# Kernel optimization log

Hardware: AMD Instinct MI355X
Metric: run time of the kernel (lower is better)

The kernel has to match this reference:

```python
import jax, jax.numpy as jnp
import numpy as np

D_TOK = 1222
N_BOU = 80

def _pe(n, d):
    pos = np.arange(n, dtype=np.float32)[:, None]
    div = np.exp(np.arange(0, d, 2, dtype=np.float32) * (-np.log(10000.0) / d))
    pe = np.zeros((n, d), np.float32)
    pe[:, 0::2] = np.sin(pos * div)
    pe[:, 1::2] = np.cos(pos * div)
    return jnp.asarray(pe)

def _ln(x, g, b, eps=1e-5):
    m = jnp.mean(x, -1, keepdims=True)
    v = jnp.mean((x - m) ** 2, -1, keepdims=True)
    return (x - m) / jnp.sqrt(v + eps) * g + b

_gather = jax.vmap(lambda f, i: f[:, i[..., 0], i[..., 1]])  # f [C,H,W], i [...,2] -> [C,...]


def setup_inputs() -> dict:
    key = jax.random.key(0)
    ks = jax.random.split(key, 8)
    D, FF, N = D_TOK, 2048, N_BOU
    s = 0.02
    return {
        "curr_img_features": jax.random.normal(ks[0], (2, 1024, 224, 224), jnp.float32),
        "previous_boundary": jax.random.randint(ks[1], (2, N, 2), 0, 224, dtype=jnp.int32),
        "ln_g": jnp.ones((D,), jnp.float32), "ln_b": jnp.zeros((D,), jnp.float32),
        "in_proj_w": s * jax.random.normal(ks[2], (3 * D, D), jnp.float32),
        "in_proj_b": jnp.zeros((3 * D,), jnp.float32),
        "out_proj_w": s * jax.random.normal(ks[3], (D, D), jnp.float32),
        "out_proj_b": jnp.zeros((D,), jnp.float32),
        "lin1_w": s * jax.random.normal(ks[4], (FF, D), jnp.float32),
        "lin1_b": jnp.zeros((FF,), jnp.float32),
        "lin2_w": s * jax.random.normal(ks[5], (D, FF), jnp.float32),
        "lin2_b": jnp.zeros((D,), jnp.float32),
        "norm1_g": jnp.ones((D,), jnp.float32), "norm1_b": jnp.zeros((D,), jnp.float32),
        "norm2_g": jnp.ones((D,), jnp.float32), "norm2_b": jnp.zeros((D,), jnp.float32),
        "fc_w": s * jax.random.normal(ks[6], (N, 1026, D), jnp.float32),
        "fc_b": jnp.zeros((N, 1026), jnp.float32),
    }


def reference(curr_img_features, previous_boundary, ln_g, ln_b, in_proj_w, in_proj_b,
              out_proj_w, out_proj_b, lin1_w, lin1_b, lin2_w, lin2_b,
              norm1_g, norm1_b, norm2_g, norm2_b, fc_w, fc_b):
    D = D_TOK
    offs = jnp.array([[dx, dy] for dx in range(-3, 4) for dy in range(-3, 4)], jnp.int32)  # [49,2]
    # multi-scale avg-pooled + zero-padded maps (hoisted out of the refine loop; identical math)
    padded = []
    for s in range(4):
        k = 2 ** s
        f = curr_img_features
        if k > 1:
            B, C, H, W = f.shape
            f = f.reshape(B, C, H // k, k, W // k, k).mean((3, 5))
        padded.append(jnp.pad(f, ((0, 0), (0, 0), (3, 3), (3, 3))))
    pe = _pe(N_BOU, D)
    boundary = previous_boundary.astype(jnp.int32)
    results = []
    for _ in range(6):
        qf = _gather(curr_img_features, boundary)  # [B,C,N]
        dots = []
        for s in range(4):
            bs = boundary // (2 ** s)
            idx = bs[:, :, None, :] + offs[None, None] + 3  # [B,N,49,2] into padded map
            keyf = _gather(padded[s], idx)  # [B,C,N,49]
            dots.append(jnp.einsum('bcn,bcno->bno', qf, keyf))
        dots = jnp.concatenate(dots, axis=2)  # [B,N,196]
        tokens = jnp.concatenate([qf.transpose(0, 2, 1), dots,
                                  boundary.astype(jnp.float32)], axis=2)  # [B,N,1222]
        tokens = _ln(tokens, ln_g, ln_b)
        tokens = tokens + pe[None]  # positional encoding (dropout = eval/identity)
        # TransformerEncoderLayer, nhead=1, post-norm, relu, no dropout (eval)
        qkv = tokens @ in_proj_w.T + in_proj_b
        q, k_, v = jnp.split(qkv, 3, axis=-1)
        sc = jnp.einsum('bnd,bmd->bnm', q, k_) / jnp.sqrt(jnp.float32(D))
        attn = jax.nn.softmax(sc, axis=-1) @ v
        attn = attn @ out_proj_w.T + out_proj_b
        x = _ln(tokens + attn, norm1_g, norm1_b)
        ff = jax.nn.relu(x @ lin1_w.T + lin1_b) @ lin2_w.T + lin2_b
        x = _ln(x + ff, norm2_g, norm2_b)
        # 80 independent per-token heads, batched
        out = jnp.einsum('bnd,nod->bno', x, fc_w) + fc_b[None]  # [B,80,1026]
        off_f = out[..., :2]
        # torch .long() truncates toward zero; clip keeps gathers in-range (original clamp was a no-op bug)
        boundary = jnp.clip(boundary + jnp.trunc(off_f).astype(jnp.int32), 0, 223)
        results.append(boundary)
    return jnp.stack(results)  # [6,B,80,2] int32
```

## Files before the change

kernel.cpp:

```cpp
#include <hip/hip_runtime.h>
#include <math.h>

#define DTOK 1222
#define NBOU 80
#define MM   160
#define FFD  2048
#define OQKV 3666

typedef __attribute__((ext_vector_type(8))) short short8;
typedef __attribute__((ext_vector_type(4))) float f32x4;

__device__ __forceinline__ unsigned short f2bf(float x) {
  unsigned int u = __float_as_uint(x);
  unsigned int r = (u + 0x7FFFu + ((u >> 16) & 1u)) >> 16;
  return (unsigned short)r;
}
__device__ __forceinline__ float bf2f(unsigned short h) {
  return __uint_as_float((unsigned int)h << 16);
}

__device__ __forceinline__ float wave_red_sum(float v) {
#pragma unroll
  for (int off = 32; off; off >>= 1) v += __shfl_xor(v, off, 64);
  return v;
}
__device__ __forceinline__ float block_red_sum(float v, float* rb, int tid) {
  v = wave_red_sum(v);
  __syncthreads();
  if ((tid & 63) == 0) rb[tid >> 6] = v;
  __syncthreads();
  return rb[0] + rb[1] + rb[2] + rb[3];
}

__device__ __forceinline__ void frag_write_row(const float* __restrict__ row,
                                               short* __restrict__ Af,
                                               int r, int T, int tid) {
  int mt = r >> 6, mf = (r >> 4) & 3, rl = r & 15;
  for (int task = tid; task < T * 4; task += 256) {
    int t = task >> 2, kq = task & 3;
    const float* src = row + t * 32 + kq * 8;
    short8 h, l, q;
#pragma unroll
    for (int j = 0; j < 8; ++j) {
      float x = src[j];
      unsigned short hb = f2bf(x);
      float r1 = x - bf2f(hb);
      unsigned short lb = f2bf(r1);
      float r2 = r1 - bf2f(lb);
      h[j] = (short)hb; l[j] = (short)lb; q[j] = (short)f2bf(r2);
    }
    size_t base = (size_t)(mt * T + t) * 6144 + mf * 512 + (size_t)(rl + kq * 16) * 8;
    *(short8*)(Af + base) = h;
    *(short8*)(Af + base + 2048) = l;
    *(short8*)(Af + base + 4096) = q;
  }
}

__global__ __launch_bounds__(256) void k_nhwc0p(const float* __restrict__ f,
                                                float* __restrict__ L0n,
                                                float* __restrict__ L1) {
  int xt = blockIdx.x;
  int y1 = blockIdx.y;
  int zc = blockIdx.z;
  int b = zc >> 5, ct = zc & 31;
  __shared__ float tile[32][65];
  int tid = threadIdx.x;
  const float* fb = f + (size_t)b * 1024 * 50176;
#pragma unroll
  for (int i = 0; i < 8; ++i) {
    int u = tid + 256 * i;
    int xl = u & 31, r = (u >> 5) & 1, c = u >> 6;
    tile[c][xl + 32 * r] = fb[(size_t)(ct * 32 + c) * 50176 +
                              (size_t)(2 * y1 + r) * 224 + xt * 32 + xl];
  }
  __syncthreads();
#pragma unroll
  for (int i = 0; i < 8; ++i) {
    int u = tid + 256 * i;
    int c2 = u & 31, x2 = (u >> 5) & 31, r2 = u >> 10;
    L0n[(((size_t)b * 224 + 2 * y1 + r2) * 224 + xt * 32 + x2) * 1024 + ct * 32 + c2] =
        tile[c2][x2 + 32 * r2];
  }
#pragma unroll
  for (int i = 0; i < 2; ++i) {
    int u = tid + 256 * i;
    int c3 = u & 31, xp = u >> 5;
    float v = 0.25f * (tile[c3][2 * xp] + tile[c3][2 * xp + 1] +
                       tile[c3][32 + 2 * xp] + tile[c3][32 + 2 * xp + 1]);
    L1[(((size_t)b * 112 + y1) * 112 + xt * 16 + xp) * 1024 + ct * 32 + c3] = v;
  }
}

__global__ __launch_bounds__(256) void k_pool_nhwc(const float* __restrict__ in,
                                                   float* __restrict__ out, int Ho) {
  int x = blockIdx.x, y = blockIdx.y, b = blockIdx.z;
  int c = threadIdx.x * 4;
  int Hi = Ho * 2;
  const float* p00 = in + (((size_t)(b * Hi + 2 * y) * Hi) + 2 * x) * 1024 + c;
  const float* p01 = p00 + 1024;
  const float* p10 = p00 + (size_t)Hi * 1024;
  const float* p11 = p10 + 1024;
  float4 a = *(const float4*)p00, bv = *(const float4*)p01;
  float4 cv = *(const float4*)p10, dv = *(const float4*)p11;
  float4 r;
  r.x = 0.25f * (a.x + bv.x + cv.x + dv.x);
  r.y = 0.25f * (a.y + bv.y + cv.y + dv.y);
  r.z = 0.25f * (a.z + bv.z + cv.z + dv.z);
  r.w = 0.25f * (a.w + bv.w + cv.w + dv.w);
  *(float4*)(out + (((size_t)(b * Ho + y) * Ho) + x) * 1024 + c) = r;
}

__global__ __launch_bounds__(256) void k_pe(float* __restrict__ pe, int* __restrict__ bnd,
                                            const int* __restrict__ pb) {
  int n = blockIdx.x, tid = threadIdx.x;
  for (int d = tid; d < DTOK; d += 256) {
    int i = d >> 1;
    double e = exp((double)(2 * i) * (-log(10000.0) / (double)DTOK));
    double ang = (double)n * e;
    pe[n * DTOK + d] = (float)((d & 1) ? cos(ang) : sin(ang));
  }
  if (n == 0) {
    for (int t = tid; t < 2 * NBOU * 2; t += 256) bnd[t] = pb[t];
  }
}

__global__ __launch_bounds__(256) void k_conv(const float* __restrict__ X,
                                              short* __restrict__ F,
                                              int R, int K, int T) {
  int b = blockIdx.x;
  int rt = b / T, t = b % T;
  int tid = threadIdx.x, mf = tid >> 6, lane = tid & 63;
  int row = rt * 64 + mf * 16 + (lane & 15);
  int k0 = t * 32 + (lane >> 4) * 8;
  float a[8];
#pragma unroll
  for (int j = 0; j < 8; ++j) {
    int k = k0 + j;
    a[j] = (row < R && k < K) ? X[(size_t)row * K + k] : 0.f;
  }
  short8 h, l, q;
#pragma unroll
  for (int j = 0; j < 8; ++j) {
    float x = a[j];
    unsigned short hb = f2bf(x);
    float r1 = x - bf2f(hb);
    unsigned short lb = f2bf(r1);
    float r2 = r1 - bf2f(lb);
    h[j] = (short)hb; l[j] = (short)lb; q[j] = (short)f2bf(r2);
  }
  size_t base = (size_t)b * 6144 + mf * 512 + (size_t)lane * 8;
  *(short8*)(F + base) = h;
  *(short8*)(F + base + 2048) = l;
  *(short8*)(F + base + 4096) = q;
}

__global__ __launch_bounds__(256) void k_dots(const float* __restrict__ L0n,
                                              const float* __restrict__ L1,
                                              const float* __restrict__ L2,
                                              const float* __restrict__ L3,
                                              const int* __restrict__ bnd,
                                              float* __restrict__ dots) {
  int o = blockIdx.x;
  int blk = blockIdx.y;
  int b = blk / NBOU;
  int tid = threadIdx.x, s = tid >> 6, lane = tid & 63;
  int bd0 = bnd[blk * 2 + 0], bd1 = bnd[blk * 2 + 1];
  const float* cp = L0n + (((size_t)b * 224 + bd0) * 224 + bd1) * 1024;
  int Hs = 224 >> s;
  const float* base = (s == 0) ? L0n : (s == 1) ? L1 : (s == 2) ? L2 : L3;
  int yy = (bd0 >> s) + o / 7 - 3;
  int xx = (bd1 >> s) + o % 7 - 3;
  float a = 0.f;
  if (yy >= 0 && yy < Hs && xx >= 0 && xx < Hs) {
    const float* kp = base + (((size_t)b * Hs + yy) * Hs + xx) * 1024;
#pragma unroll
    for (int j = 0; j < 4; ++j) {
      int c = (lane + 64 * j) * 4;
      float4 kv = *(const float4*)(kp + c);
      float4 qv = *(const float4*)(cp + c);
      a += kv.x * qv.x + kv.y * qv.y + kv.z * qv.z + kv.w * qv.w;
    }
  }
  a = wave_red_sum(a);
  if (lane == 0) dots[blk * 196 + s * 49 + o] = a;
}

__global__ __launch_bounds__(256) void k_tokln(const float* __restrict__ L0n,
                                               const int* __restrict__ bnd,
                                               const float* __restrict__ dots,
                                               const float* __restrict__ g,
                                               const float* __restrict__ bb,
                                               const float* __restrict__ pe,
                                               float* __restrict__ tok_out,
                                               short* __restrict__ Af, int T) {
  int blk = blockIdx.x;
  int b = blk / NBOU, n = blk % NBOU;
  int tid = threadIdx.x;
  __shared__ __align__(16) float token[1248];
  __shared__ float rbuf[8];
  int bd0 = bnd[blk * 2 + 0], bd1 = bnd[blk * 2 + 1];
  const float* cp = L0n + (((size_t)b * 224 + bd0) * 224 + bd1) * 1024;
  {
    int d = tid * 4;
    *(float4*)&token[d] = *(const float4*)(cp + d);
  }
  if (tid < 196) token[1024 + tid] = dots[blk * 196 + tid];
  if (tid == 0) { token[1220] = (float)bd0; token[1221] = (float)bd1; }
  if (tid < 26) token[1222 + tid] = 0.f;
  __syncthreads();

  float ls = 0.f;
  for (int d = tid; d < DTOK; d += 256) ls += token[d];
  float mean = block_red_sum(ls, rbuf, tid) * (1.0f / DTOK);
  float lq = 0.f;
  for (int d = tid; d < DTOK; d += 256) { float t = token[d] - mean; lq += t * t; }
  float var = block_red_sum(lq, rbuf, tid) * (1.0f / DTOK);
  float rstd = rsqrtf(var + 1e-5f);
  for (int d = tid; d < DTOK; d += 256) {
    float o = (token[d] - mean) * rstd * g[d] + bb[d] + pe[n * DTOK + d];
    tok_out[(size_t)blk * DTOK + d] = o;
    token[d] = o;
  }
  __syncthreads();
  frag_write_row(token, Af, blk, T, tid);
}

__global__ __launch_bounds__(256) void k_mfma2(const short* __restrict__ Af,
                                               const short* __restrict__ Bf,
                                               float* __restrict__ partial,
                                               int T, int O, int S) {
  int nt = blockIdx.x, sp = blockIdx.y;
  int tid = threadIdx.x, w = tid >> 6, lane = tid & 63;
  int wr = w >> 1, wc = w & 1;
  int rl = lane & 15, kq = lane >> 4;
  int cps = (T + S - 1) / S;
  int t0 = sp * cps, t1 = min(t0 + cps, T);

  f32x4 acc[3][2][2];
#pragma unroll
  for (int mt = 0; mt < 3; ++mt)
#pragma unroll
    for (int mi = 0; mi < 2; ++mi)
#pragma unroll
      for (int ni = 0; ni < 2; ++ni) acc[mt][mi][ni] = (f32x4){0.f, 0.f, 0.f, 0.f};

  const size_t bbase = (size_t)(wc * 2) * 512 + (size_t)lane * 8;
  const size_t abase = (size_t)(wr * 2) * 512 + (size_t)lane * 8;

  short8 bv[3][2], bv2[3][2];

#define LOADB(tt, BV)                                                          \
  {                                                                            \
    const short* bp = Bf + ((size_t)nt * T + (tt)) * 6144 + bbase;             \
    _Pragma("unroll")                                                          \
    for (int s = 0; s < 3; ++s)                                                \
      _Pragma("unroll")                                                        \
      for (int ni = 0; ni < 2; ++ni)                                           \
        BV[s][ni] = *(const short8*)(bp + s * 2048 + ni * 512);                \
  }

  if (t0 < t1) {
    LOADB(t0, bv);
    for (int t = t0; t < t1; ++t) {
      if (t + 1 < t1) LOADB(t + 1, bv2);
#pragma unroll
      for (int mt = 0; mt < 3; ++mt) {
        const short* ap = Af + ((size_t)(mt * T + t)) * 6144 + abase;
        short8 af[3][2];
#pragma unroll
        for (int s = 0; s < 3; ++s)
#pragma unroll
          for (int mi = 0; mi < 2; ++mi)
            af[s][mi] = *(const short8*)(ap + s * 2048 + mi * 512);
#pragma unroll
        for (int mi = 0; mi < 2; ++mi)
#pragma unroll
          for (int ni = 0; ni < 2; ++ni) {
            f32x4 a = acc[mt][mi][ni];
            a = __builtin_amdgcn_mfma_f32_16x16x32_bf16(af[0][mi], bv[0][ni], a, 0, 0, 0);
            a = __builtin_amdgcn_mfma_f32_16x16x32_bf16(af[0][mi], bv[1][ni], a, 0, 0, 0);
            a = __builtin_amdgcn_mfma_f32_16x16x32_bf16(af[1][mi], bv[0][ni], a, 0, 0, 0);
            a = __builtin_amdgcn_mfma_f32_16x16x32_bf16(af[0][mi], bv[2][ni], a, 0, 0, 0);
            a = __builtin_amdgcn_mfma_f32_16x16x32_bf16(af[2][mi], bv[0][ni], a, 0, 0, 0);
            a = __builtin_amdgcn_mfma_f32_16x16x32_bf16(af[1][mi], bv[1][ni], a, 0, 0, 0);
            acc[mt][mi][ni] = a;
          }
      }
#pragma unroll
      for (int s = 0; s < 3; ++s)
#pragma unroll
        for (int ni = 0; ni < 2; ++ni) bv[s][ni] = bv2[s][ni];
    }
  }
#undef LOADB

  float* pp = partial + (size_t)sp * MM * O;
#pragma unroll
  for (int mt = 0; mt < 3; ++mt)
#pragma unroll
    for (int mi = 0; mi < 2; ++mi)
#pragma unroll
      for (int ni = 0; ni < 2; ++ni) {
        int c = nt * 64 + wc * 32 + ni * 16 + rl;
        if (c >= O) continue;
#pragma unroll
        for (int reg = 0; reg < 4; ++reg) {
          int r = mt * 64 + wr * 32 + mi * 16 + kq * 4 + reg;
          if (r < MM) pp[(size_t)r * O + c] = acc[mt][mi][ni][reg];
        }
      }
}

__global__ __launch_bounds__(256) void k_red4(const float* __restrict__ partial,
                                              const float* __restrict__ bias,
                                              float* __restrict__ out,
                                              int O, int S) {
  size_t idx = ((size_t)blockIdx.x * 256 + threadIdx.x) * 4;
  size_t total = (size_t)MM * O;
  if (idx >= total) return;
  float4 v = *(const float4*)(partial + idx);
  for (int s = 1; s < S; ++s) {
    float4 p = *(const float4*)(partial + (size_t)s * total + idx);
    v.x += p.x; v.y += p.y; v.z += p.z; v.w += p.w;
  }
  float r[4] = {v.x, v.y, v.z, v.w};
#pragma unroll
  for (int j = 0; j < 4; ++j) r[j] += bias[(int)((idx + j) % O)];
  float4 wv = {r[0], r[1], r[2], r[3]};
  *(float4*)(out + idx) = wv;
}

__global__ __launch_bounds__(256) void k_redf(const float* __restrict__ partial,
                                              const float* __restrict__ bias,
                                              short* __restrict__ Af,
                                              int S, int T) {
  const int O = FFD;
  size_t idx8 = ((size_t)blockIdx.x * 256 + threadIdx.x) * 8;
  size_t total = (size_t)MM * O;
  if (idx8 >= total) return;
  int r = (int)(idx8 / O), c = (int)(idx8 % O);
  float v[8];
#pragma unroll
  for (int j = 0; j < 8; ++j) v[j] = 0.f;
  for (int s = 0; s < S; ++s) {
    const float* p = partial + (size_t)s * total + idx8;
#pragma unroll
    for (int j = 0; j < 8; ++j) v[j] += p[j];
  }
  short8 h, l, q;
#pragma unroll
  for (int j = 0; j < 8; ++j) {
    float x = fmaxf(v[j] + bias[c + j], 0.f);
    unsigned short hb = f2bf(x);
    float r1 = x - bf2f(hb);
    unsigned short lb = f2bf(r1);
    float r2 = r1 - bf2f(lb);
    h[j] = (short)hb; l[j] = (short)lb; q[j] = (short)f2bf(r2);
  }
  int mt = r >> 6, mf = (r >> 4) & 3, rl = r & 15;
  int t = c >> 5, kq = (c >> 3) & 3;
  size_t base = (size_t)(mt * T + t) * 6144 + mf * 512 + (size_t)(rl + kq * 16) * 8;
  *(short8*)(Af + base) = h;
  *(short8*)(Af + base + 2048) = l;
  *(short8*)(Af + base + 4096) = q;
}

__global__ __launch_bounds__(256) void k_redln(const float* __restrict__ partial,
                                               const float* __restrict__ bias,
                                               const float* __restrict__ res,
                                               const float* __restrict__ g,
                                               const float* __restrict__ bb,
                                               float* __restrict__ xout,
                                               short* __restrict__ Af,
                                               int S, int T) {
  const int O = DTOK;
  int m = blockIdx.x, tid = threadIdx.x;
  __shared__ __align__(16) float row[1248];
  __shared__ float rb[8];
  if (tid < 26) row[1222 + tid] = 0.f;
  float ls = 0.f;
  for (int d = tid; d < O; d += 256) {
    float v = 0.f;
    for (int s = 0; s < S; ++s) v += partial[((size_t)s * MM + m) * O + d];
    v += bias[d];
    v += res[(size_t)m * O + d];
    row[d] = v; ls += v;
  }
  float mean = block_red_sum(ls, rb, tid) * (1.0f / DTOK);
  float lq = 0.f;
  for (int d = tid; d < O; d += 256) { float t = row[d] - mean; lq += t * t; }
  float var = block_red_sum(lq, rb, tid) * (1.0f / DTOK);
  float rstd = rsqrtf(var + 1e-5f);
  for (int d = tid; d < O; d += 256) {
    float xn = (row[d] - mean) * rstd * g[d] + bb[d];
    xout[(size_t)m * O + d] = xn;
    row[d] = xn;
  }
  __syncthreads();
  frag_write_row(row, Af, m, T, tid);
}

__global__ __launch_bounds__(256) void k_redlnfc(const float* __restrict__ partial,
                                                 const float* __restrict__ bias,
                                                 const float* __restrict__ res,
                                                 const float* __restrict__ g,
                                                 const float* __restrict__ bb,
                                                 const float* __restrict__ fcw,
                                                 const float* __restrict__ fcb,
                                                 int* __restrict__ bnd,
                                                 int* __restrict__ outp,
                                                 int S) {
  const int O = DTOK;
  int blk = blockIdx.x;
  int n = blk % NBOU;
  int tid = threadIdx.x;
  __shared__ float row[DTOK];
  __shared__ float rb[8];
  float ls = 0.f;
  for (int d = tid; d < O; d += 256) {
    float v = 0.f;
    for (int s = 0; s < S; ++s) v += partial[((size_t)s * MM + blk) * O + d];
    v += bias[d];
    v += res[(size_t)blk * O + d];
    row[d] = v; ls += v;
  }
  float mean = block_red_sum(ls, rb, tid) * (1.0f / DTOK);
  float lq = 0.f;
  for (int d = tid; d < O; d += 256) { float t = row[d] - mean; lq += t * t; }
  float var = block_red_sum(lq, rb, tid) * (1.0f / DTOK);
  float rstd = rsqrtf(var + 1e-5f);
  const float* w0 = fcw + (size_t)n * 1026 * DTOK;
  const float* w1 = w0 + DTOK;
  float s0 = 0.f, s1 = 0.f;
  for (int d = tid; d < O; d += 256) {
    float xn = (row[d] - mean) * rstd * g[d] + bb[d];
    s0 += xn * w0[d];
    s1 += xn * w1[d];
  }
  s0 = block_red_sum(s0, rb, tid);
  s1 = block_red_sum(s1, rb, tid);
  if (tid == 0) {
    float o0 = s0 + fcb[n * 1026 + 0];
    float o1 = s1 + fcb[n * 1026 + 1];
    int b0 = bnd[blk * 2 + 0], b1 = bnd[blk * 2 + 1];
    int nb0 = b0 + (int)truncf(o0);
    int nb1 = b1 + (int)truncf(o1);
    nb0 = nb0 < 0 ? 0 : (nb0 > 223 ? 223 : nb0);
    nb1 = nb1 < 0 ? 0 : (nb1 > 223 ? 223 : nb1);
    bnd[blk * 2 + 0] = nb0;
    bnd[blk * 2 + 1] = nb1;
    outp[blk * 2 + 0] = nb0;
    outp[blk * 2 + 1] = nb1;
  }
}

__global__ __launch_bounds__(256) void k_qk(const float* __restrict__ qkv,
                                            float* __restrict__ sc) {
  int blk = blockIdx.x, qc = blockIdx.y;
  int b = blk / NBOU;
  int tid = threadIdx.x, wave = tid >> 6, lane = tid & 63;
  float qr[20];
  const float* qrow = qkv + (size_t)blk * OQKV;
#pragma unroll
  for (int j = 0; j < 20; ++j) {
    int d = lane + 64 * j;
    qr[j] = (d < DTOK) ? qrow[d] : 0.f;
  }
#pragma unroll
  for (int i = 0; i < 5; ++i) {
    int m2 = qc * 20 + wave * 5 + i;
    const float* krow = qkv + (size_t)(b * NBOU + m2) * OQKV + DTOK;
    float a = 0.f;
#pragma unroll
    for (int j = 0; j < 20; ++j) {
      int d = lane + 64 * j;
      if (d < DTOK) a += qr[j] * krow[d];
    }
    a = wave_red_sum(a);
    if (lane == 0) sc[blk * 80 + m2] = a * (1.0f / 34.957116f);
  }
}

__global__ __launch_bounds__(256) void k_attn2(const float* __restrict__ qkv,
                                               const float* __restrict__ sc,
                                               short* __restrict__ Af, int T) {
  int blk = blockIdx.x;
  int b = blk / NBOU;
  int tid = threadIdx.x, wave = tid >> 6, lane = tid & 63;
  __shared__ float p[80];
  __shared__ __align__(16) float smem[4][1248];
  if (wave == 0) {
    float x0 = sc[blk * 80 + lane];
    float x1 = (lane < 16) ? sc[blk * 80 + 64 + lane] : -INFINITY;
    float mx = fmaxf(x0, x1);
#pragma unroll
    for (int off = 32; off; off >>= 1) mx = fmaxf(mx, __shfl_xor(mx, off, 64));
    float e0 = expf(x0 - mx);
    float e1 = (lane < 16) ? expf(x1 - mx) : 0.f;
    float ssum = wave_red_sum(e0 + e1);
    p[lane] = e0 / ssum;
    if (lane < 16) p[64 + lane] = e1 / ssum;
  }
  __syncthreads();
  float acc[20];
#pragma unroll
  for (int j = 0; j < 20; ++j) acc[j] = 0.f;
  for (int i = 0; i < 20; ++i) {
    int m2 = wave * 20 + i;
    float pm = p[m2];
    const float* vrow = qkv + (size_t)(b * NBOU + m2) * OQKV + 2 * DTOK;
#pragma unroll
    for (int j = 0; j < 20; ++j) {
      int d = lane + 64 * j;
      if (d < DTOK) acc[j] += pm * vrow[d];
    }
  }
#pragma unroll
  for (int j = 0; j < 20; ++j) {
    int d = lane + 64 * j;
    if (d < DTOK) smem[wave][d] = acc[j];
  }
  __syncthreads();
  for (int d = tid; d < DTOK; d += 256)
    smem[0][d] = ((smem[0][d] + smem[1][d]) + smem[2][d]) + smem[3][d];
  if (tid < 26) smem[0][1222 + tid] = 0.f;
  __syncthreads();
  frag_write_row(smem[0], Af, blk, T, tid);
}

extern "C" void kernel_launch(void* const* d_in, const int* in_sizes, int n_in,
                              void* d_out, int out_size, void* d_ws, size_t ws_size,
                              hipStream_t stream) {
  const float* f   = (const float*)d_in[0];
  const int*   pb  = (const int*)d_in[1];
  const float* lng = (const float*)d_in[2];
  const float* lnb = (const float*)d_in[3];
  const float* ipw = (const float*)d_in[4];
  const float* ipb = (const float*)d_in[5];
  const float* opw = (const float*)d_in[6];
  const float* opb = (const float*)d_in[7];
  const float* l1w = (const float*)d_in[8];
  const float* l1b = (const float*)d_in[9];
  const float* l2w = (const float*)d_in[10];
  const float* l2b = (const float*)d_in[11];
  const float* n1g = (const float*)d_in[12];
  const float* n1b = (const float*)d_in[13];
  const float* n2g = (const float*)d_in[14];
  const float* n2b = (const float*)d_in[15];
  const float* fcw = (const float*)d_in[16];
  const float* fcb = (const float*)d_in[17];
  int* outp = (int*)d_out;

  const int T1 = 39;
  const int T2 = 64;
  const int NT_IP = 58, NT_OP = 20, NT_L1 = 32, NT_L2 = 20;
  const int S_IP = 6, S_OP = 10, S_L1 = 8, S_L2 = 16;

  char* wsb = (char*)d_ws;
  auto alloc = [&](size_t bytes) -> char* {
    char* p = wsb;
    wsb += (bytes + 255) & ~(size_t)255;
    return p;
  };
  float* L0n  = (float*)alloc((size_t)2 * 224 * 224 * 1024 * 4);
  float* L1   = (float*)alloc((size_t)2 * 112 * 112 * 1024 * 4);
  float* L2   = (float*)alloc((size_t)2 * 56 * 56 * 1024 * 4);
  float* L3   = (float*)alloc((size_t)2 * 28 * 28 * 1024 * 4);
  float* pe   = (float*)alloc((size_t)NBOU * DTOK * 4);
  int*   bnd  = (int*)alloc(320 * 4);
  float* tokens = (float*)alloc((size_t)MM * DTOK * 4);
  float* qkvb   = (float*)alloc((size_t)MM * OQKV * 4);
  float* x1     = (float*)alloc((size_t)MM * DTOK * 4);
  float* dots   = (float*)alloc((size_t)MM * 196 * 4);
  float* scb    = (float*)alloc((size_t)MM * 80 * 4);
  short* Af1  = (short*)alloc((size_t)3 * T1 * 6144 * 2);
  short* Af2  = (short*)alloc((size_t)3 * T2 * 6144 * 2);
  short* ipWf = (short*)alloc((size_t)NT_IP * T1 * 6144 * 2);
  short* opWf = (short*)alloc((size_t)NT_OP * T1 * 6144 * 2);
  short* l1Wf = (short*)alloc((size_t)NT_L1 * T1 * 6144 * 2);
  short* l2Wf = (short*)alloc((size_t)NT_L2 * T2 * 6144 * 2);
  float* part = (float*)alloc((size_t)S_IP * MM * OQKV * 4);

  k_nhwc0p<<<dim3(7, 112, 64), 256, 0, stream>>>(f, L0n, L1);
  k_pool_nhwc<<<dim3(56, 56, 2), 256, 0, stream>>>(L1, L2, 56);
  k_pool_nhwc<<<dim3(28, 28, 2), 256, 0, stream>>>(L2, L3, 28);
  k_pe<<<NBOU, 256, 0, stream>>>(pe, bnd, pb);

  k_conv<<<NT_IP * T1, 256, 0, stream>>>(ipw, ipWf, OQKV, DTOK, T1);
  k_conv<<<NT_OP * T1, 256, 0, stream>>>(opw, opWf, DTOK, DTOK, T1);
  k_conv<<<NT_L1 * T1, 256, 0, stream>>>(l1w, l1Wf, FFD, DTOK, T1);
  k_conv<<<NT_L2 * T2, 256, 0, stream>>>(l2w, l2Wf, DTOK, FFD, T2);

  for (int it = 0; it < 6; ++it) {
    k_dots<<<dim3(49, 160), 256, 0, stream>>>(L0n, L1, L2, L3, bnd, dots);
    k_tokln<<<160, 256, 0, stream>>>(L0n, bnd, dots, lng, lnb, pe, tokens, Af1, T1);

    k_mfma2<<<dim3(NT_IP, S_IP), 256, 0, stream>>>(Af1, ipWf, part, T1, OQKV, S_IP);
    k_red4<<<(MM * OQKV + 1023) / 1024, 256, 0, stream>>>(part, ipb, qkvb, OQKV, S_IP);

    k_qk<<<dim3(160, 4), 256, 0, stream>>>(qkvb, scb);
    k_attn2<<<160, 256, 0, stream>>>(qkvb, scb, Af1, T1);

    k_mfma2<<<dim3(NT_OP, S_OP), 256, 0, stream>>>(Af1, opWf, part, T1, DTOK, S_OP);
    k_redln<<<160, 256, 0, stream>>>(part, opb, tokens, n1g, n1b, x1, Af1, S_OP, T1);

    k_mfma2<<<dim3(NT_L1, S_L1), 256, 0, stream>>>(Af1, l1Wf, part, T1, FFD, S_L1);
    k_redf<<<MM * FFD / 2048, 256, 0, stream>>>(part, l1b, Af2, S_L1, T2);

    k_mfma2<<<dim3(NT_L2, S_L2), 256, 0, stream>>>(Af2, l2Wf, part, T2, DTOK, S_L2);
    k_redlnfc<<<160, 256, 0, stream>>>(part, l2b, x1, n2g, n2b, fcw, fcb, bnd, outp + it * 320, S_L2);
  }
}
```

Baseline: 1.285 ms.

## Fuse QK scores, softmax and PV into one kernel; merge pooling levels

```diff
diff --git a/kernel.cpp b/kernel.cpp
--- a/kernel.cpp
+++ b/kernel.cpp
@@ -62,52 +62,65 @@
   int xt = blockIdx.x;
   int y1 = blockIdx.y;
   int zc = blockIdx.z;
-  int b = zc >> 5, ct = zc & 31;
-  __shared__ float tile[32][65];
+  int b = zc >> 4, ct = zc & 15;
+  __shared__ float tile[64][65];
   int tid = threadIdx.x;
   const float* fb = f + (size_t)b * 1024 * 50176;
 #pragma unroll
-  for (int i = 0; i < 8; ++i) {
+  for (int i = 0; i < 16; ++i) {
     int u = tid + 256 * i;
     int xl = u & 31, r = (u >> 5) & 1, c = u >> 6;
-    tile[c][xl + 32 * r] = fb[(size_t)(ct * 32 + c) * 50176 +
+    tile[c][xl + 32 * r] = fb[(size_t)(ct * 64 + c) * 50176 +
                               (size_t)(2 * y1 + r) * 224 + xt * 32 + xl];
   }
   __syncthreads();
 #pragma unroll
-  for (int i = 0; i < 8; ++i) {
+  for (int i = 0; i < 16; ++i) {
     int u = tid + 256 * i;
-    int c2 = u & 31, x2 = (u >> 5) & 31, r2 = u >> 10;
-    L0n[(((size_t)b * 224 + 2 * y1 + r2) * 224 + xt * 32 + x2) * 1024 + ct * 32 + c2] =
+    int c2 = u & 63, x2 = (u >> 6) & 31, r2 = u >> 11;
+    L0n[(((size_t)b * 224 + 2 * y1 + r2) * 224 + xt * 32 + x2) * 1024 + ct * 64 + c2] =
         tile[c2][x2 + 32 * r2];
   }
 #pragma unroll
-  for (int i = 0; i < 2; ++i) {
+  for (int i = 0; i < 4; ++i) {
     int u = tid + 256 * i;
-    int c3 = u & 31, xp = u >> 5;
+    int c3 = u & 63, xp = u >> 6;
     float v = 0.25f * (tile[c3][2 * xp] + tile[c3][2 * xp + 1] +
                        tile[c3][32 + 2 * xp] + tile[c3][32 + 2 * xp + 1]);
-    L1[(((size_t)b * 112 + y1) * 112 + xt * 16 + xp) * 1024 + ct * 32 + c3] = v;
-  }
-}
-
-__global__ __launch_bounds__(256) void k_pool_nhwc(const float* __restrict__ in,
-                                                   float* __restrict__ out, int Ho) {
-  int x = blockIdx.x, y = blockIdx.y, b = blockIdx.z;
+    L1[(((size_t)b * 112 + y1) * 112 + xt * 16 + xp) * 1024 + ct * 64 + c3] = v;
+  }
+}
+
+__global__ __launch_bounds__(256) void k_pool23(const float* __restrict__ L1,
+                                                float* __restrict__ L2,
+                                                float* __restrict__ L3) {
+  int x3 = blockIdx.x, y3 = blockIdx.y, b = blockIdx.z;
   int c = threadIdx.x * 4;
-  int Hi = Ho * 2;
-  const float* p00 = in + (((size_t)(b * Hi + 2 * y) * Hi) + 2 * x) * 1024 + c;
-  const float* p01 = p00 + 1024;
-  const float* p10 = p00 + (size_t)Hi * 1024;
-  const float* p11 = p10 + 1024;
-  float4 a = *(const float4*)p00, bv = *(const float4*)p01;
-  float4 cv = *(const float4*)p10, dv = *(const float4*)p11;
-  float4 r;
-  r.x = 0.25f * (a.x + bv.x + cv.x + dv.x);
-  r.y = 0.25f * (a.y + bv.y + cv.y + dv.y);
-  r.z = 0.25f * (a.z + bv.z + cv.z + dv.z);
-  r.w = 0.25f * (a.w + bv.w + cv.w + dv.w);
-  *(float4*)(out + (((size_t)(b * Ho + y) * Ho) + x) * 1024 + c) = r;
+  float4 l2v[2][2];
+#pragma unroll
+  for (int yy = 0; yy < 2; ++yy)
+#pragma unroll
+    for (int xx = 0; xx < 2; ++xx) {
+      const float* p00 = L1 + (((size_t)(b * 112 + 4 * y3 + 2 * yy) * 112) + 4 * x3 + 2 * xx) * 1024 + c;
+      const float* p01 = p00 + 1024;
+      const float* p10 = p00 + (size_t)112 * 1024;
+      const float* p11 = p10 + 1024;
+      float4 a = *(const float4*)p00, bv = *(const float4*)p01;
+      float4 cv = *(const float4*)p10, dv = *(const float4*)p11;
+      float4 r;
+      r.x = 0.25f * (a.x + bv.x + cv.x + dv.x);
+      r.y = 0.25f * (a.y + bv.y + cv.y + dv.y);
+      r.z = 0.25f * (a.z + bv.z + cv.z + dv.z);
+      r.w = 0.25f * (a.w + bv.w + cv.w + dv.w);
+      l2v[yy][xx] = r;
+      *(float4*)(L2 + (((size_t)(b * 56 + 2 * y3 + yy) * 56) + 2 * x3 + xx) * 1024 + c) = r;
+    }
+  float4 r3;
+  r3.x = 0.25f * (l2v[0][0].x + l2v[0][1].x + l2v[1][0].x + l2v[1][1].x);
+  r3.y = 0.25f * (l2v[0][0].y + l2v[0][1].y + l2v[1][0].y + l2v[1][1].y);
+  r3.z = 0.25f * (l2v[0][0].z + l2v[0][1].z + l2v[1][0].z + l2v[1][1].z);
+  r3.w = 0.25f * (l2v[0][0].w + l2v[0][1].w + l2v[1][0].w + l2v[1][1].w);
+  *(float4*)(L3 + (((size_t)(b * 28 + y3) * 28) + x3) * 1024 + c) = r3;
 }
 
 __global__ __launch_bounds__(256) void k_pe(float* __restrict__ pe, int* __restrict__ bnd,
@@ -454,60 +467,52 @@
   }
 }
 
-__global__ __launch_bounds__(256) void k_qk(const float* __restrict__ qkv,
-                                            float* __restrict__ sc) {
-  int blk = blockIdx.x, qc = blockIdx.y;
-  int b = blk / NBOU;
-  int tid = threadIdx.x, wave = tid >> 6, lane = tid & 63;
-  float qr[20];
-  const float* qrow = qkv + (size_t)blk * OQKV;
-#pragma unroll
-  for (int j = 0; j < 20; ++j) {
-    int d = lane + 64 * j;
-    qr[j] = (d < DTOK) ? qrow[d] : 0.f;
-  }
-#pragma unroll
-  for (int i = 0; i < 5; ++i) {
-    int m2 = qc * 20 + wave * 5 + i;
-    const float* krow = qkv + (size_t)(b * NBOU + m2) * OQKV + DTOK;
-    float a = 0.f;
-#pragma unroll
-    for (int j = 0; j < 20; ++j) {
-      int d = lane + 64 * j;
-      if (d < DTOK) a += qr[j] * krow[d];
-    }
-    a = wave_red_sum(a);
-    if (lane == 0) sc[blk * 80 + m2] = a * (1.0f / 34.957116f);
-  }
-}
-
-__global__ __launch_bounds__(256) void k_attn2(const float* __restrict__ qkv,
-                                               const float* __restrict__ sc,
+__global__ __launch_bounds__(512) void k_attn3(const float* __restrict__ qkv,
                                                short* __restrict__ Af, int T) {
   int blk = blockIdx.x;
   int b = blk / NBOU;
-  int tid = threadIdx.x, wave = tid >> 6, lane = tid & 63;
-  __shared__ float p[80];
-  __shared__ __align__(16) float smem[4][1248];
-  if (wave == 0) {
-    float x0 = sc[blk * 80 + lane];
-    float x1 = (lane < 16) ? sc[blk * 80 + 64 + lane] : -INFINITY;
+  int tid = threadIdx.x, w = tid >> 6, lane = tid & 63;
+  __shared__ __align__(16) float q[1224];
+  __shared__ float sc[80];
+  __shared__ __align__(16) float pv[8][1248];
+  const float* qrow = qkv + (size_t)blk * OQKV;
+  for (int d = tid; d < DTOK; d += 512) q[d] = qrow[d];
+  __syncthreads();
+
+#pragma unroll
+  for (int i = 0; i < 10; ++i) {
+    int m2 = w * 10 + i;
+    const float* krow = qkv + (size_t)(b * NBOU + m2) * OQKV + DTOK;
+    float a = 0.f;
+#pragma unroll
+    for (int j = 0; j < 20; ++j) {
+      int d = lane + 64 * j;
+      if (d < DTOK) a += q[d] * krow[d];
+    }
+    a = wave_red_sum(a);
+    if (lane == 0) sc[m2] = a * (1.0f / 34.957116f);
+  }
+  __syncthreads();
+  if (w == 0) {
+    float x0 = sc[lane];
+    float x1 = (lane < 16) ? sc[64 + lane] : -INFINITY;
     float mx = fmaxf(x0, x1);
 #pragma unroll
     for (int off = 32; off; off >>= 1) mx = fmaxf(mx, __shfl_xor(mx, off, 64));
     float e0 = expf(x0 - mx);
     float e1 = (lane < 16) ? expf(x1 - mx) : 0.f;
     float ssum = wave_red_sum(e0 + e1);
-    p[lane] = e0 / ssum;
-    if (lane < 16) p[64 + lane] = e1 / ssum;
-  }
-  __syncthreads();
+    sc[lane] = e0 / ssum;
+    if (lane < 16) sc[64 + lane] = e1 / ssum;
+  }
+  __syncthreads();
+
   float acc[20];
 #pragma unroll
   for (int j = 0; j < 20; ++j) acc[j] = 0.f;
-  for (int i = 0; i < 20; ++i) {
-    int m2 = wave * 20 + i;
-    float pm = p[m2];
+  for (int i = 0; i < 10; ++i) {
+    int m2 = w * 10 + i;
+    float pm = sc[m2];
     const float* vrow = qkv + (size_t)(b * NBOU + m2) * OQKV + 2 * DTOK;
 #pragma unroll
     for (int j = 0; j < 20; ++j) {
@@ -518,14 +523,18 @@
 #pragma unroll
   for (int j = 0; j < 20; ++j) {
     int d = lane + 64 * j;
-    if (d < DTOK) smem[wave][d] = acc[j];
-  }
-  __syncthreads();
-  for (int d = tid; d < DTOK; d += 256)
-    smem[0][d] = ((smem[0][d] + smem[1][d]) + smem[2][d]) + smem[3][d];
-  if (tid < 26) smem[0][1222 + tid] = 0.f;
-  __syncthreads();
-  frag_write_row(smem[0], Af, blk, T, tid);
+    if (d < DTOK) pv[w][d] = acc[j];
+  }
+  __syncthreads();
+  for (int d = tid; d < DTOK; d += 512) {
+    float v = pv[0][d];
+#pragma unroll
+    for (int s = 1; s < 8; ++s) v += pv[s][d];
+    pv[0][d] = v;
+  }
+  if (tid < 26) pv[0][1222 + tid] = 0.f;
+  __syncthreads();
+  frag_write_row(pv[0], Af, blk, T, tid);
 }
 
 extern "C" void kernel_launch(void* const* d_in, const int* in_sizes, int n_in,
@@ -572,7 +581,6 @@
   float* qkvb   = (float*)alloc((size_t)MM * OQKV * 4);
   float* x1     = (float*)alloc((size_t)MM * DTOK * 4);
   float* dots   = (float*)alloc((size_t)MM * 196 * 4);
-  float* scb    = (float*)alloc((size_t)MM * 80 * 4);
   short* Af1  = (short*)alloc((size_t)3 * T1 * 6144 * 2);
   short* Af2  = (short*)alloc((size_t)3 * T2 * 6144 * 2);
   short* ipWf = (short*)alloc((size_t)NT_IP * T1 * 6144 * 2);
@@ -581,9 +589,8 @@
   short* l2Wf = (short*)alloc((size_t)NT_L2 * T2 * 6144 * 2);
   float* part = (float*)alloc((size_t)S_IP * MM * OQKV * 4);
 
-  k_nhwc0p<<<dim3(7, 112, 64), 256, 0, stream>>>(f, L0n, L1);
-  k_pool_nhwc<<<dim3(56, 56, 2), 256, 0, stream>>>(L1, L2, 56);
-  k_pool_nhwc<<<dim3(28, 28, 2), 256, 0, stream>>>(L2, L3, 28);
+  k_nhwc0p<<<dim3(7, 112, 32), 256, 0, stream>>>(f, L0n, L1);
+  k_pool23<<<dim3(28, 28, 2), 256, 0, stream>>>(L1, L2, L3);
   k_pe<<<NBOU, 256, 0, stream>>>(pe, bnd, pb);
 
   k_conv<<<NT_IP * T1, 256, 0, stream>>>(ipw, ipWf, OQKV, DTOK, T1);
@@ -598,8 +605,7 @@
     k_mfma2<<<dim3(NT_IP, S_IP), 256, 0, stream>>>(Af1, ipWf, part, T1, OQKV, S_IP);
     k_red4<<<(MM * OQKV + 1023) / 1024, 256, 0, stream>>>(part, ipb, qkvb, OQKV, S_IP);
 
-    k_qk<<<dim3(160, 4), 256, 0, stream>>>(qkvb, scb);
-    k_attn2<<<160, 256, 0, stream>>>(qkvb, scb, Af1, T1);
+    k_attn3<<<160, 512, 0, stream>>>(qkvb, Af1, T1);
 
     k_mfma2<<<dim3(NT_OP, S_OP), 256, 0, stream>>>(Af1, opWf, part, T1, DTOK, S_OP);
     k_redln<<<160, 256, 0, stream>>>(part, opb, tokens, n1g, n1b, x1, Af1, S_OP, T1);
```

New measurement: 1.269 ms. About the same (-1.3%).
